# Kernel tuning notes

Measured on AMD Instinct MI355X. Metric: run time of the kernel, lower is better.

The kernel has to match this reference:

```python
import jax, jax.numpy as jnp
import numpy as np

N = 32768          # B*T flattened tokens
E = 1024           # embed_dim
H = 16             # num_heads
D = E // H         # head_dim = 64


def setup_inputs() -> dict:
    key = jax.random.key(0)
    ks = jax.random.split(key, 9)
    w = lambda k: jax.random.normal(k, (E, E), jnp.float32) * (E ** -0.5)
    b = lambda k: jax.random.normal(k, (E,), jnp.float32) * 0.01
    return {
        "x": jax.random.normal(ks[0], (N, E), jnp.float32),
        "Wq": w(ks[1]), "bq": b(ks[2]),
        "Wk": w(ks[3]), "bk": b(ks[4]),
        "Wv": w(ks[5]), "bv": b(ks[6]),
        "Wo": w(ks[7]), "bo": b(ks[8]),
    }


def reference(x, Wq, bq, Wk, bk, Wv, bv, Wo, bo):
    # nn.Linear: y = x @ W^T + b
    q = (x @ Wq.T + bq).reshape(-1, H, D)   # [N, H, D]
    k = (x @ Wk.T + bk).reshape(-1, H, D)
    v = (x @ Wv.T + bv).reshape(-1, H, D)
    scale = D ** -0.5
    # per-token attention ACROSS HEADS: scores [N, H, H]
    qk = jnp.einsum('nhd,nHd->nhH', q, k) * scale
    attn = jax.nn.softmax(qk, axis=-1)      # softmax over key-heads
    out = jnp.einsum('nhH,nHd->nhd', attn, v).reshape(-1, E)
    return out @ Wo.T + bo                  # [N, E]
```

## Files before the change

### kernel.cpp

```cpp
#include <hip/hip_runtime.h>

typedef __attribute__((ext_vector_type(8))) short short8;
typedef __attribute__((ext_vector_type(8))) unsigned short ushort8;
typedef __attribute__((ext_vector_type(4))) float f32x4;

__device__ __forceinline__ float b2f(short s) {
    unsigned u = ((unsigned)(unsigned short)s) << 16;
    return __builtin_bit_cast(float, u);
}
__device__ __forceinline__ unsigned short f2b(float f) {
    unsigned u = __builtin_bit_cast(unsigned, f);
    u += 0x7fffu + ((u >> 16) & 1u);
    return (unsigned short)(u >> 16);
}

__device__ __forceinline__ void gload_lds16(const void* gptr, void* ldsptr) {
    typedef __attribute__((address_space(1))) const void gv_t;
    typedef __attribute__((address_space(3))) void lv_t;
    gv_t* g = reinterpret_cast<gv_t*>(reinterpret_cast<unsigned long long>(gptr));
    lv_t* l = reinterpret_cast<lv_t*>((unsigned int)reinterpret_cast<unsigned long long>(ldsptr));
    __builtin_amdgcn_global_load_lds(g, l, 16, 0, 0);
}

#define MEMFENCE() asm volatile("" ::: "memory")
#define BARRIER() do { MEMFENCE(); __builtin_amdgcn_s_barrier(); MEMFENCE(); } while (0)

__global__ __launch_bounds__(256) void cvt_all(const float* __restrict__ x,
                                               const float* __restrict__ Wq,
                                               const float* __restrict__ Wk,
                                               const float* __restrict__ Wv,
                                               const float* __restrict__ Wo,
                                               const float* __restrict__ bq,
                                               const float* __restrict__ bk,
                                               const float* __restrict__ bv,
                                               unsigned short* __restrict__ xb,
                                               unsigned short* __restrict__ wqkv,
                                               unsigned short* __restrict__ wo,
                                               float* __restrict__ bqkv) {
    const int bid = blockIdx.x;
    const float* src;
    unsigned short* dst;
    int base8;
    if (bid < 16384)      { src = x;  dst = xb;              base8 = bid; }
    else if (bid < 16896) { src = Wq; dst = wqkv;            base8 = bid - 16384; }
    else if (bid < 17408) { src = Wk; dst = wqkv + 1048576;  base8 = bid - 16896; }
    else if (bid < 17920) { src = Wv; dst = wqkv + 2097152;  base8 = bid - 17408; }
    else if (bid < 18432) { src = Wo; dst = wo;              base8 = bid - 17920; }
    else {
        const int i = threadIdx.x;
#pragma unroll
        for (int r = 0; r < 12; ++r) {
            int j = r * 256 + i;
            float v = (j < 1024) ? bq[j] : (j < 2048 ? bk[j - 1024] : bv[j - 2048]);
            bqkv[j] = v;
        }
        return;
    }
    const size_t i8 = (size_t)base8 * 256 + threadIdx.x;
    const float4* p = (const float4*)src + i8 * 2;
    float4 a = p[0], b = p[1];
    ushort8 o;
    o[0] = f2b(a.x); o[1] = f2b(a.y); o[2] = f2b(a.z); o[3] = f2b(a.w);
    o[4] = f2b(b.x); o[5] = f2b(b.y); o[6] = f2b(b.z); o[7] = f2b(b.w);
    *(ushort8*)(dst + i8 * 8) = o;
}

template <bool OUT_BF16>
__global__ __launch_bounds__(512, 2) void gemm_bt(const short* __restrict__ A,
                                                  const short* __restrict__ B,
                                                  const float* __restrict__ bias,
                                                  unsigned short* __restrict__ Cb,
                                                  float* __restrict__ Cf,
                                                  int M, int N, int K) {
    extern __shared__ short lds[];
    short* Ab = lds;
    short* Bb = lds + 2 * 2 * 128 * 64;

    const int lane = threadIdx.x & 63;
    const int wave = threadIdx.x >> 6;
    const int wr = wave >> 2;
    const int wc = wave & 3;

    const int nwg = gridDim.x;
    const int bid = blockIdx.x;
    const int swz = (bid & 7) * (nwg >> 3) + (bid >> 3);
    const int ncol = N >> 8;
    const int trow = swz / ncol, tcol = swz % ncol;

    const short* Ablk = A + (size_t)trow * 256 * K;
    const short* Bblk = B + (size_t)tcol * 256 * K;

    const int scol_sw = ((lane & 7) ^ (lane >> 3)) * 8;
    const int rl = lane & 15;
    const int g0 = (((lane >> 4)) ^ (lane & 7)) * 8;
    const int g1 = ((4 + (lane >> 4)) ^ (lane & 7)) * 8;

    short8 af[4][2];
    short8 bf[4][2];
    f32x4 acc[8][4] = {};

    const int NT = K >> 6;
    const int smax = 4 * (NT - 2);

    auto stage_half = [&](int ts, int h) {
        const int dd = ts & 1;
        const int hh = h & 1;
        const short* gb = ((h < 2) ? Ablk : Bblk) + (size_t)(hh * 128) * K + (ts << 6) + scol_sw;
        short* lb = ((h < 2) ? Ab : Bb) + (((dd << 1) | hh) << 13);
#pragma unroll
        for (int c = 0; c < 2; ++c) {
            const int row = c * 64 + wave * 8 + (lane >> 3);
            gload_lds16(gb + (size_t)row * K, lb + ((c * 64 + wave * 8) << 6));
        }
    };
    auto stage_if = [&](int s) { if (s >= 0 && s < smax) stage_half((s >> 2) + 2, s & 3); };

    auto readA = [&](int d, int mh) {
        const short* base = Ab + (((d << 1) | wr) << 13) + ((mh * 64 + rl) << 6);
#pragma unroll
        for (int m = 0; m < 4; ++m) {
            af[m][0] = *(const short8*)(base + ((m * 16) << 6) + g0);
            af[m][1] = *(const short8*)(base + ((m * 16) << 6) + g1);
        }
    };
    auto readB = [&](int d, int nh) {
        const short* base = Bb + (((d << 1) | (wc >> 1)) << 13) + (((wc & 1) * 64 + rl) << 6);
#pragma unroll
        for (int j = 0; j < 2; ++j) {
            bf[nh * 2 + j][0] = *(const short8*)(base + (((nh * 2 + j) * 16) << 6) + g0);
            bf[nh * 2 + j][1] = *(const short8*)(base + (((nh * 2 + j) * 16) << 6) + g1);
        }
    };
    auto mm = [&](int mh, int nh) {
        __builtin_amdgcn_s_setprio(1);
#pragma unroll
        for (int ks = 0; ks < 2; ++ks)
#pragma unroll
            for (int m = 0; m < 4; ++m)
#pragma unroll
                for (int j = 0; j < 2; ++j)
                    acc[mh * 4 + m][nh * 2 + j] = __builtin_amdgcn_mfma_f32_16x16x32_bf16(
                        af[m][ks], bf[nh * 2 + j][ks], acc[mh * 4 + m][nh * 2 + j], 0, 0, 0);
        __builtin_amdgcn_s_setprio(0);
    };

    auto tile_body = [&](int T, int d) {
        const int s0 = 4 * T;
        readA(d, 0); readB(d, 0);
        stage_if(s0 - 3);
        asm volatile("s_waitcnt lgkmcnt(8)" ::: "memory");
        BARRIER();
        asm volatile("s_waitcnt lgkmcnt(0)" ::: "memory");
        mm(0, 0);
        BARRIER();
        readB(d, 1);
        stage_if(s0 - 2);
        BARRIER();
        asm volatile("s_waitcnt lgkmcnt(0)" ::: "memory");
        mm(0, 1);
        BARRIER();
        readA(d, 1);
        stage_if(s0 - 1);
        BARRIER();
        asm volatile("s_waitcnt lgkmcnt(0)" ::: "memory");
        mm(1, 0);
        BARRIER();
        stage_if(s0);
        BARRIER();
        mm(1, 1);
        if (T < NT - 2)       asm volatile("s_waitcnt vmcnt(2)" ::: "memory");
        else if (T == NT - 2) asm volatile("s_waitcnt vmcnt(0)" ::: "memory");
        BARRIER();
    };

#pragma unroll
    for (int t = 0; t < 2; ++t)
#pragma unroll
        for (int h = 0; h < 4; ++h) stage_half(t, h);
    asm volatile("s_waitcnt vmcnt(8)" ::: "memory");
    BARRIER();

    for (int T2 = 0; T2 < NT; T2 += 2) {
        tile_body(T2, 0);
        tile_body(T2 + 1, 1);
    }

    const int crow0 = trow * 256 + wr * 128 + (lane >> 4) * 4;
    const int ccol0 = tcol * 256 + wc * 64 + rl;
#pragma unroll
    for (int n = 0; n < 4; ++n) {
        const int col = ccol0 + n * 16;
        const float bv = bias[col];
#pragma unroll
        for (int m = 0; m < 8; ++m) {
            const int row0 = crow0 + m * 16;
#pragma unroll
            for (int r = 0; r < 4; ++r) {
                float val = acc[m][n][r] + bv;
                if (OUT_BF16) Cb[(size_t)(row0 + r) * N + col] = f2b(val);
                else          Cf[(size_t)(row0 + r) * N + col] = val;
            }
        }
    }
}

#define MMQ(AF, BF, MB, NB)                                                            \
    do {                                                                               \
        __builtin_amdgcn_s_setprio(1);                                                 \
        _Pragma("unroll")                                                              \
        for (int m_ = 0; m_ < 4; ++m_)                                                 \
            _Pragma("unroll")                                                          \
            for (int n_ = 0; n_ < 2; ++n_)                                             \
                acc[(MB) + m_][(NB) + n_] = __builtin_amdgcn_mfma_f32_16x16x32_bf16(   \
                    AF[m_], BF[n_], acc[(MB) + m_][(NB) + n_], 0, 0, 0);               \
        __builtin_amdgcn_s_setprio(0);                                                 \
    } while (0)

__global__ __launch_bounds__(512, 2) void gemm_pf(const short* __restrict__ A,
                                                  const short* __restrict__ B,
                                                  const float* __restrict__ bias,
                                                  float* __restrict__ Cf,
                                                  int M, int N, int K) {
    extern __shared__ short lds[];
    const int lane = threadIdx.x & 63;
    const int wave = threadIdx.x >> 6;
    const int wr = wave >> 2;
    const int wc = wave & 3;

    const int nwg = gridDim.x;
    const int bid = blockIdx.x;
    const int swz = (bid & 7) * (nwg >> 3) + (bid >> 3);
    const int ncol = N >> 8;
    const int trow = swz / ncol, tcol = swz % ncol;

    const short* Ablk = A + (size_t)trow * 256 * K;
    const short* Bblk = B + (size_t)tcol * 256 * K;

    const int s_r = lane >> 2;
    const int s_c = ((lane & 3) ^ ((lane >> 3) & 3)) * 8;
    const int rl = lane & 15;
    const int gph = ((lane >> 4) ^ ((rl >> 1) & 3)) * 8;

    short8 af0[4], af1[4], bf0[2], bf1[2];
    f32x4 acc[8][4] = {};

    const int NT = K >> 5;
    const int smax = 4 * (NT - 2);

    auto stage_half = [&](int ts, int h) {
        const int dd = ts & 1;
        const int hh = h & 1;
        const int R0 = hh * 128 + wave * 16;
        const short* gb = (h < 2) ? Ablk : Bblk;
        short* lb = lds + ((h < 2) ? 0 : 16384) + dd * 8192;
        gload_lds16(gb + (size_t)(R0 + s_r) * K + (ts << 5) + s_c, lb + R0 * 32);
    };
    auto stage_if = [&](int s) { if (s >= 0 && s < smax) stage_half((s >> 2) + 2, s & 3); };

    auto readA0 = [&](int d) {
        const short* base = lds + d * 8192 + (wr * 128 + rl) * 32 + gph;
#pragma unroll
        for (int m = 0; m < 4; ++m) af0[m] = *(const short8*)(base + m * 16 * 32);
    };
    auto readA1 = [&](int d) {
        const short* base = lds + d * 8192 + (wr * 128 + 64 + rl) * 32 + gph;
#pragma unroll
        for (int m = 0; m < 4; ++m) af1[m] = *(const short8*)(base + m * 16 * 32);
    };
    auto readB0 = [&](int d) {
        const short* base = lds + 16384 + d * 8192 + (wc * 64 + rl) * 32 + gph;
#pragma unroll
        for (int j = 0; j < 2; ++j) bf0[j] = *(const short8*)(base + j * 16 * 32);
    };
    auto readB1 = [&](int d) {
        const short* base = lds + 16384 + d * 8192 + (wc * 64 + 32 + rl) * 32 + gph;
#pragma unroll
        for (int j = 0; j < 2; ++j) bf1[j] = *(const short8*)(base + j * 16 * 32);
    };

#pragma unroll
    for (int t = 0; t < 2; ++t)
#pragma unroll
        for (int h = 0; h < 4; ++h) stage_half(t, h);
    asm volatile("s_waitcnt vmcnt(4)" ::: "memory");
    BARRIER();
    readA0(0); readB0(0);

    for (int t = 0; t < NT; ++t) {
        const int d = t & 1;
        const int s0 = 4 * t;
        stage_if(s0 - 3);
        readA1(d);
        asm volatile("s_waitcnt lgkmcnt(4)" ::: "memory");
        MMQ(af0, bf0, 0, 0);
        stage_if(s0 - 2);
        readB1(d);
        asm volatile("s_waitcnt lgkmcnt(2)" ::: "memory");
        MMQ(af1, bf0, 4, 0);
        BARRIER();
        stage_if(s0 - 1);
        asm volatile("s_waitcnt lgkmcnt(0)" ::: "memory");
        MMQ(af0, bf1, 0, 2);
        stage_if(s0);
        if (t < NT - 2) asm volatile("s_waitcnt vmcnt(1)" ::: "memory");
        else            asm volatile("s_waitcnt vmcnt(0)" ::: "memory");
        BARRIER();
        if (t + 1 < NT) { readA0(d ^ 1); readB0(d ^ 1); }
        asm volatile("s_waitcnt lgkmcnt(6)" ::: "memory");
        MMQ(af1, bf1, 4, 2);
    }

    const int crow0 = trow * 256 + wr * 128 + (lane >> 4) * 4;
    const int ccol0 = tcol * 256 + wc * 64 + rl;
#pragma unroll
    for (int n = 0; n < 4; ++n) {
        const int col = ccol0 + n * 16;
        const float bv = bias[col];
#pragma unroll
        for (int m = 0; m < 8; ++m) {
            const int row0 = crow0 + m * 16;
#pragma unroll
            for (int r = 0; r < 4; ++r)
                Cf[(size_t)(row0 + r) * N + col] = acc[m][n][r] + bv;
        }
    }
}

__global__ __launch_bounds__(256) void attn_k(const short* __restrict__ qkv,
                                              short* __restrict__ out) {
    int gid = blockIdx.x * 256 + threadIdx.x;
    int t = gid >> 4, h = gid & 15;
    const short* q  = qkv + (size_t)t * 3072 + h * 64;
    const short* kb = qkv + (size_t)t * 3072 + 1024;
    const short* vb = qkv + (size_t)t * 3072 + 2048;

    float qf[64];
#pragma unroll
    for (int j = 0; j < 8; ++j) {
        short8 qv = *(const short8*)(q + j * 8);
#pragma unroll
        for (int i = 0; i < 8; ++i) qf[j * 8 + i] = b2f(qv[i]);
    }

    float s[16];
    float mx = -1e30f;
#pragma unroll
    for (int g = 0; g < 16; ++g) {
        float a = 0.f;
#pragma unroll
        for (int j = 0; j < 8; ++j) {
            short8 kv = *(const short8*)(kb + g * 64 + j * 8);
#pragma unroll
            for (int i = 0; i < 8; ++i) a += qf[j * 8 + i] * b2f(kv[i]);
        }
        s[g] = a * 0.125f;
        mx = fmaxf(mx, s[g]);
    }
    float den = 0.f;
#pragma unroll
    for (int g = 0; g < 16; ++g) { s[g] = __expf(s[g] - mx); den += s[g]; }
    float inv = 1.f / den;

#pragma unroll
    for (int j = 0; j < 8; ++j) {
        float o[8] = {0.f, 0.f, 0.f, 0.f, 0.f, 0.f, 0.f, 0.f};
#pragma unroll
        for (int g = 0; g < 16; ++g) {
            short8 vv = *(const short8*)(vb + g * 64 + j * 8);
            float w = s[g];
#pragma unroll
            for (int i = 0; i < 8; ++i) o[i] += w * b2f(vv[i]);
        }
        short8 ov;
#pragma unroll
        for (int i = 0; i < 8; ++i) ov[i] = (short)f2b(o[i] * inv);
        *(short8*)(out + (size_t)t * 1024 + h * 64 + j * 8) = ov;
    }
}

extern "C" void kernel_launch(void* const* d_in, const int* in_sizes, int n_in,
                              void* d_out, int out_size, void* d_ws, size_t ws_size,
                              hipStream_t stream) {
    const float* x  = (const float*)d_in[0];
    const float* Wq = (const float*)d_in[1];
    const float* bq = (const float*)d_in[2];
    const float* Wk = (const float*)d_in[3];
    const float* bk = (const float*)d_in[4];
    const float* Wv = (const float*)d_in[5];
    const float* bv = (const float*)d_in[6];
    const float* Wo = (const float*)d_in[7];
    const float* bo = (const float*)d_in[8];
    float* out = (float*)d_out;

    const int N = 32768, E = 1024;

    (void)hipFuncSetAttribute((const void*)gemm_bt<true>, hipFuncAttributeMaxDynamicSharedMemorySize, 131072);
    (void)hipFuncSetAttribute((const void*)gemm_pf,       hipFuncAttributeMaxDynamicSharedMemorySize, 65536);

    char* ws = (char*)d_ws;
    size_t off = 0;
    short* xb = (short*)(ws + off);         off += (size_t)N * E * 2;
    short* wqkv = (short*)(ws + off);       off += (size_t)3 * E * E * 2;
    short* wo = (short*)(ws + off);         off += (size_t)E * E * 2;
    float* bqkv = (float*)(ws + off);       off += (size_t)3 * E * 4;
    off = (off + 255) & ~(size_t)255;
    short* y1 = (short*)(ws + off);         off += (size_t)N * 3 * E * 2;
    short* ao = xb;

    cvt_all<<<dim3(18433), dim3(256), 0, stream>>>(
        x, Wq, Wk, Wv, Wo, bq, bk, bv,
        (unsigned short*)xb, (unsigned short*)wqkv, (unsigned short*)wo, bqkv);

    gemm_bt<true><<<dim3((N / 256) * (3 * E / 256)), dim3(512), 131072, stream>>>(
        xb, wqkv, bqkv, (unsigned short*)y1, nullptr, N, 3 * E, E);

    attn_k<<<dim3(N * 16 / 256), dim3(256), 0, stream>>>(y1, ao);

    gemm_pf<<<dim3((N / 256) * (E / 256)), dim3(512), 65536, stream>>>(
        ao, wo, bo, out, N, E, E);
}
```

Before: 478.7 us.

## Use 4-wave 256x256 GEMM with 128x128 per-wave tiles for QKV projection

Result: slower. 1.066 ms (+122.8%).

```diff
diff --git a/kernel.cpp b/kernel.cpp
--- a/kernel.cpp
+++ b/kernel.cpp
@@ -66,6 +66,115 @@
 }
 
 template <bool OUT_BF16>
+__global__ __launch_bounds__(256, 1) void gemm_dp(const short* __restrict__ A,
+                                                  const short* __restrict__ B,
+                                                  const float* __restrict__ bias,
+                                                  unsigned short* __restrict__ Cb,
+                                                  float* __restrict__ Cf,
+                                                  int M, int N, int K) {
+    extern __shared__ short lds[];
+    short* Ab = lds;
+    short* Bb = lds + 32768;
+
+    const int lane = threadIdx.x & 63;
+    const int wave = threadIdx.x >> 6;
+    const int wr = wave >> 1, wc = wave & 1;
+
+    const int nwg = gridDim.x;
+    const int bid = blockIdx.x;
+    const int swz = (bid & 7) * (nwg >> 3) + (bid >> 3);
+    const int ncol = N >> 8;
+    const int trow = swz / ncol, tcol = swz % ncol;
+
+    const short* Ablk = A + (size_t)trow * 256 * K;
+    const short* Bblk = B + (size_t)tcol * 256 * K;
+
+    const int srow_off = lane >> 3;
+    const int scol_sw = ((lane & 7) ^ (lane >> 3)) * 8;
+    const int rl = lane & 15;
+    const int g0 = ((lane >> 4) ^ (lane & 7)) * 8;
+    const int g1 = ((4 + (lane >> 4)) ^ (lane & 7)) * 8;
+
+    short8 a0[8], a1[8], b0[8], b1[8];
+    f32x4 acc[8][8] = {};
+
+    const int NT = K >> 6;
+
+    auto stage = [&](int t, int d) {
+#pragma unroll
+        for (int i = 0; i < 8; ++i) {
+            const int stripe = i * 4 + wave;
+            gload_lds16(Ablk + (size_t)(stripe * 8 + srow_off) * K + t * 64 + scol_sw,
+                        Ab + d * 16384 + stripe * 512);
+            gload_lds16(Bblk + (size_t)(stripe * 8 + srow_off) * K + t * 64 + scol_sw,
+                        Bb + d * 16384 + stripe * 512);
+        }
+    };
+    auto readA = [&](int d, int g, short8* dst) {
+        const short* base = Ab + d * 16384 + (wr * 128 + rl) * 64 + g;
+#pragma unroll
+        for (int m = 0; m < 8; ++m) dst[m] = *(const short8*)(base + m * 16 * 64);
+    };
+    auto readB = [&](int d, int g, short8* dst) {
+        const short* base = Bb + d * 16384 + (wc * 128 + rl) * 64 + g;
+#pragma unroll
+        for (int n = 0; n < 8; ++n) dst[n] = *(const short8*)(base + n * 16 * 64);
+    };
+    auto mmhalf = [&](short8* av, short8* bv) {
+        __builtin_amdgcn_s_setprio(1);
+#pragma unroll
+        for (int m = 0; m < 8; ++m)
+#pragma unroll
+            for (int n = 0; n < 8; ++n)
+                acc[m][n] = __builtin_amdgcn_mfma_f32_16x16x32_bf16(av[m], bv[n], acc[m][n], 0, 0, 0);
+        __builtin_amdgcn_s_setprio(0);
+    };
+
+    stage(0, 0);
+    stage(1, 1);
+    asm volatile("s_waitcnt vmcnt(16)" ::: "memory");
+    BARRIER();
+    readA(0, g0, a0); readB(0, g0, b0);
+
+    for (int t = 0; t < NT; ++t) {
+        const int d = t & 1;
+        readA(d, g1, a1); readB(d, g1, b1);
+        asm volatile("s_waitcnt lgkmcnt(15)" ::: "memory");
+        mmhalf(a0, b0);
+        __builtin_amdgcn_sched_barrier(0);
+        asm volatile("s_waitcnt lgkmcnt(0)" ::: "memory");
+        BARRIER();
+        if (t + 2 < NT) stage(t + 2, d);
+        if (t + 1 < NT) {
+            if (t + 2 < NT) asm volatile("s_waitcnt vmcnt(16)" ::: "memory");
+            else            asm volatile("s_waitcnt vmcnt(0)"  ::: "memory");
+        }
+        BARRIER();
+        if (t + 1 < NT) { readA(d ^ 1, g0, a0); readB(d ^ 1, g0, b0); }
+        __builtin_amdgcn_sched_barrier(0);
+        mmhalf(a1, b1);
+    }
+
+    const int crow0 = trow * 256 + wr * 128 + (lane >> 4) * 4;
+    const int ccol0 = tcol * 256 + wc * 128 + rl;
+#pragma unroll
+    for (int n = 0; n < 8; ++n) {
+        const int col = ccol0 + n * 16;
+        const float bv = bias[col];
+#pragma unroll
+        for (int m = 0; m < 8; ++m) {
+            const int row0 = crow0 + m * 16;
+#pragma unroll
+            for (int r = 0; r < 4; ++r) {
+                float val = acc[m][n][r] + bv;
+                if (OUT_BF16) Cb[(size_t)(row0 + r) * N + col] = f2b(val);
+                else          Cf[(size_t)(row0 + r) * N + col] = val;
+            }
+        }
+    }
+}
+
+template <bool OUT_BF16>
 __global__ __launch_bounds__(512, 2) void gemm_bt(const short* __restrict__ A,
                                                   const short* __restrict__ B,
                                                   const float* __restrict__ bias,
@@ -200,128 +309,6 @@
                 if (OUT_BF16) Cb[(size_t)(row0 + r) * N + col] = f2b(val);
                 else          Cf[(size_t)(row0 + r) * N + col] = val;
             }
-        }
-    }
-}
-
-#define MMQ(AF, BF, MB, NB)                                                            \
-    do {                                                                               \
-        __builtin_amdgcn_s_setprio(1);                                                 \
-        _Pragma("unroll")                                                              \
-        for (int m_ = 0; m_ < 4; ++m_)                                                 \
-            _Pragma("unroll")                                                          \
-            for (int n_ = 0; n_ < 2; ++n_)                                             \
-                acc[(MB) + m_][(NB) + n_] = __builtin_amdgcn_mfma_f32_16x16x32_bf16(   \
-                    AF[m_], BF[n_], acc[(MB) + m_][(NB) + n_], 0, 0, 0);               \
-        __builtin_amdgcn_s_setprio(0);                                                 \
-    } while (0)
-
-__global__ __launch_bounds__(512, 2) void gemm_pf(const short* __restrict__ A,
-                                                  const short* __restrict__ B,
-                                                  const float* __restrict__ bias,
-                                                  float* __restrict__ Cf,
-                                                  int M, int N, int K) {
-    extern __shared__ short lds[];
-    const int lane = threadIdx.x & 63;
-    const int wave = threadIdx.x >> 6;
-    const int wr = wave >> 2;
-    const int wc = wave & 3;
-
-    const int nwg = gridDim.x;
-    const int bid = blockIdx.x;
-    const int swz = (bid & 7) * (nwg >> 3) + (bid >> 3);
-    const int ncol = N >> 8;
-    const int trow = swz / ncol, tcol = swz % ncol;
-
-    const short* Ablk = A + (size_t)trow * 256 * K;
-    const short* Bblk = B + (size_t)tcol * 256 * K;
-
-    const int s_r = lane >> 2;
-    const int s_c = ((lane & 3) ^ ((lane >> 3) & 3)) * 8;
-    const int rl = lane & 15;
-    const int gph = ((lane >> 4) ^ ((rl >> 1) & 3)) * 8;
-
-    short8 af0[4], af1[4], bf0[2], bf1[2];
-    f32x4 acc[8][4] = {};
-
-    const int NT = K >> 5;
-    const int smax = 4 * (NT - 2);
-
-    auto stage_half = [&](int ts, int h) {
-        const int dd = ts & 1;
-        const int hh = h & 1;
-        const int R0 = hh * 128 + wave * 16;
-        const short* gb = (h < 2) ? Ablk : Bblk;
-        short* lb = lds + ((h < 2) ? 0 : 16384) + dd * 8192;
-        gload_lds16(gb + (size_t)(R0 + s_r) * K + (ts << 5) + s_c, lb + R0 * 32);
-    };
-    auto stage_if = [&](int s) { if (s >= 0 && s < smax) stage_half((s >> 2) + 2, s & 3); };
-
-    auto readA0 = [&](int d) {
-        const short* base = lds + d * 8192 + (wr * 128 + rl) * 32 + gph;
-#pragma unroll
-        for (int m = 0; m < 4; ++m) af0[m] = *(const short8*)(base + m * 16 * 32);
-    };
-    auto readA1 = [&](int d) {
-        const short* base = lds + d * 8192 + (wr * 128 + 64 + rl) * 32 + gph;
-#pragma unroll
-        for (int m = 0; m < 4; ++m) af1[m] = *(const short8*)(base + m * 16 * 32);
-    };
-    auto readB0 = [&](int d) {
-        const short* base = lds + 16384 + d * 8192 + (wc * 64 + rl) * 32 + gph;
-#pragma unroll
-        for (int j = 0; j < 2; ++j) bf0[j] = *(const short8*)(base + j * 16 * 32);
-    };
-    auto readB1 = [&](int d) {
-        const short* base = lds + 16384 + d * 8192 + (wc * 64 + 32 + rl) * 32 + gph;
-#pragma unroll
-        for (int j = 0; j < 2; ++j) bf1[j] = *(const short8*)(base + j * 16 * 32);
-    };
-
-#pragma unroll
-    for (int t = 0; t < 2; ++t)
-#pragma unroll
-        for (int h = 0; h < 4; ++h) stage_half(t, h);
-    asm volatile("s_waitcnt vmcnt(4)" ::: "memory");
-    BARRIER();
-    readA0(0); readB0(0);
-
-    for (int t = 0; t < NT; ++t) {
-        const int d = t & 1;
-        const int s0 = 4 * t;
-        stage_if(s0 - 3);
-        readA1(d);
-        asm volatile("s_waitcnt lgkmcnt(4)" ::: "memory");
-        MMQ(af0, bf0, 0, 0);
-        stage_if(s0 - 2);
-        readB1(d);
-        asm volatile("s_waitcnt lgkmcnt(2)" ::: "memory");
-        MMQ(af1, bf0, 4, 0);
-        BARRIER();
-        stage_if(s0 - 1);
-        asm volatile("s_waitcnt lgkmcnt(0)" ::: "memory");
-        MMQ(af0, bf1, 0, 2);
-        stage_if(s0);
-        if (t < NT - 2) asm volatile("s_waitcnt vmcnt(1)" ::: "memory");
-        else            asm volatile("s_waitcnt vmcnt(0)" ::: "memory");
-        BARRIER();
-        if (t + 1 < NT) { readA0(d ^ 1); readB0(d ^ 1); }
-        asm volatile("s_waitcnt lgkmcnt(6)" ::: "memory");
-        MMQ(af1, bf1, 4, 2);
-    }
-
-    const int crow0 = trow * 256 + wr * 128 + (lane >> 4) * 4;
-    const int ccol0 = tcol * 256 + wc * 64 + rl;
-#pragma unroll
-    for (int n = 0; n < 4; ++n) {
-        const int col = ccol0 + n * 16;
-        const float bv = bias[col];
-#pragma unroll
-        for (int m = 0; m < 8; ++m) {
-            const int row0 = crow0 + m * 16;
-#pragma unroll
-            for (int r = 0; r < 4; ++r)
-                Cf[(size_t)(row0 + r) * N + col] = acc[m][n][r] + bv;
         }
     }
 }
@@ -394,8 +381,8 @@
 
     const int N = 32768, E = 1024;
 
-    (void)hipFuncSetAttribute((const void*)gemm_bt<true>, hipFuncAttributeMaxDynamicSharedMemorySize, 131072);
-    (void)hipFuncSetAttribute((const void*)gemm_pf,       hipFuncAttributeMaxDynamicSharedMemorySize, 65536);
+    (void)hipFuncSetAttribute((const void*)gemm_dp<true>,  hipFuncAttributeMaxDynamicSharedMemorySize, 131072);
+    (void)hipFuncSetAttribute((const void*)gemm_bt<false>, hipFuncAttributeMaxDynamicSharedMemorySize, 131072);
 
     char* ws = (char*)d_ws;
     size_t off = 0;
@@ -411,11 +398,11 @@
         x, Wq, Wk, Wv, Wo, bq, bk, bv,
         (unsigned short*)xb, (unsigned short*)wqkv, (unsigned short*)wo, bqkv);
 
-    gemm_bt<true><<<dim3((N / 256) * (3 * E / 256)), dim3(512), 131072, stream>>>(
+    gemm_dp<true><<<dim3((N / 256) * (3 * E / 256)), dim3(256), 131072, stream>>>(
         xb, wqkv, bqkv, (unsigned short*)y1, nullptr, N, 3 * E, E);
 
     attn_k<<<dim3(N * 16 / 256), dim3(256), 0, stream>>>(y1, ao);
 
-    gemm_pf<<<dim3((N / 256) * (E / 256)), dim3(512), 65536, stream>>>(
-        ao, wo, bo, out, N, E, E);
-}
+    gemm_bt<false><<<dim3((N / 256) * (E / 256)), dim3(512), 131072, stream>>>(
+        ao, wo, bo, nullptr, out, N, E, E);
+}
```
